# Performance work log

Hardware: AMD Instinct MI355X
Metric: run time of the kernel (lower is better)

Reference implementation:

```python
import jax, jax.numpy as jnp
import numpy as np
from jax.ops import segment_sum, segment_max

N, E, F, HID, HEADS, OUT, G = 50000, 800000, 128, 64, 2, 128, 50
EPS = 1e-5


def setup_inputs() -> dict:
    key = jax.random.key(0)
    ks = iter(jax.random.split(key, 80))
    def p(*shape):
        return jax.random.normal(next(ks), shape, jnp.float32) * 0.1
    inp = {}
    inp['x'] = jax.random.normal(next(ks), (N, F), jnp.float32)
    inp['edge_index'] = jax.random.randint(next(ks), (2, E), 0, N)
    inp['batch'] = jnp.repeat(jnp.arange(G), N // G)
    dims = [(F, HID), (HID, HID), (HID, OUT)]
    for i, (a, b) in enumerate(dims):
        inp[f'gcn_W{i}'] = p(a, b); inp[f'gcn_b{i}'] = jnp.zeros((b,), jnp.float32)
    for i in range(2):
        inp[f'gcn_bn_g{i}'] = jnp.ones((HID,), jnp.float32); inp[f'gcn_bn_b{i}'] = jnp.zeros((HID,), jnp.float32)
    gat_dims = [(F, HEADS, HID), (HEADS * HID, HEADS, HID), (HEADS * HID, 1, OUT)]
    for i, (a, h, c) in enumerate(gat_dims):
        inp[f'gat_W{i}'] = p(a, h * c)
        inp[f'gat_as{i}'] = p(h, c)
        inp[f'gat_ad{i}'] = p(h, c)
        inp[f'gat_b{i}'] = jnp.zeros((h * c if i < 2 else c,), jnp.float32)
    for i in range(2):
        inp[f'gat_bn_g{i}'] = jnp.ones((HEADS * HID,), jnp.float32); inp[f'gat_bn_b{i}'] = jnp.zeros((HEADS * HID,), jnp.float32)
    for i, (a, b) in enumerate(dims):
        inp[f'sage_Wl{i}'] = p(a, b); inp[f'sage_Wr{i}'] = p(a, b); inp[f'sage_b{i}'] = jnp.zeros((b,), jnp.float32)
    for i in range(2):
        inp[f'sage_bn_g{i}'] = jnp.ones((HID,), jnp.float32); inp[f'sage_bn_b{i}'] = jnp.zeros((HID,), jnp.float32)
    inp['fus_W'] = p(3 * OUT, OUT); inp['fus_b'] = jnp.zeros((OUT,), jnp.float32)
    return inp


def _bn(x, g, b):
    m = x.mean(0)
    v = x.var(0)
    return (x - m) * jax.lax.rsqrt(v + EPS) * g + b


def _pool(x, batch):
    s = segment_sum(x, batch, num_segments=G)
    c = segment_sum(jnp.ones((x.shape[0], 1), x.dtype), batch, num_segments=G)
    return s / jnp.maximum(c, 1.0)


def _with_self_loops(src, dst):
    loop = jnp.arange(N)
    return jnp.concatenate([src, loop]), jnp.concatenate([dst, loop])


def _gcn_conv(x, W, b, src, dst):
    # PyG GCNConv: linear, add self loops, symmetric D^-1/2 normalization, scatter-add at dst
    h = x @ W
    srcf, dstf = _with_self_loops(src, dst)
    deg = segment_sum(jnp.ones(srcf.shape[0], x.dtype), dstf, num_segments=N)
    dis = jnp.where(deg > 0, jax.lax.rsqrt(jnp.maximum(deg, 1.0)), 0.0)
    norm = dis[srcf] * dis[dstf]
    return segment_sum(h[srcf] * norm[:, None], dstf, num_segments=N) + b


def _gat_conv(x, W, a_s, a_d, b, src, dst, concat):
    # PyG GATConv: per-head additive attention, leaky_relu(0.2), softmax over incoming edges
    Hh, C = a_s.shape
    h = (x @ W).reshape(N, Hh, C)
    al_src = (h * a_s).sum(-1)  # [N,H]
    al_dst = (h * a_d).sum(-1)  # [N,H]
    srcf, dstf = _with_self_loops(src, dst)
    e = jax.nn.leaky_relu(al_src[srcf] + al_dst[dstf], 0.2)  # [E+N,H]
    m = segment_max(e, dstf, num_segments=N)
    ex = jnp.exp(e - m[dstf])
    denom = segment_sum(ex, dstf, num_segments=N)
    alpha = ex / (denom[dstf] + 1e-16)
    out = segment_sum(h[srcf] * alpha[:, :, None], dstf, num_segments=N)  # [N,H,C]
    out = out.reshape(N, Hh * C) if concat else out.mean(1)
    return out + b


def _sage_conv(x, Wl, Wr, b, src, dst):
    # PyG SAGEConv(mean): lin_l(mean of neighbors) + lin_r(x)
    s = segment_sum(x[src], dst, num_segments=N)
    cnt = segment_sum(jnp.ones((E, 1), x.dtype), dst, num_segments=N)
    mean = s / jnp.maximum(cnt, 1.0)
    return mean @ Wl + x @ Wr + b


def _forward(x, edge_index, batch,
             gcn_W0, gcn_b0, gcn_W1, gcn_b1, gcn_W2, gcn_b2,
             gcn_bn_g0, gcn_bn_b0, gcn_bn_g1, gcn_bn_b1,
             gat_W0, gat_as0, gat_ad0, gat_b0,
             gat_W1, gat_as1, gat_ad1, gat_b1,
             gat_W2, gat_as2, gat_ad2, gat_b2,
             gat_bn_g0, gat_bn_b0, gat_bn_g1, gat_bn_b1,
             sage_Wl0, sage_Wr0, sage_b0,
             sage_Wl1, sage_Wr1, sage_b1,
             sage_Wl2, sage_Wr2, sage_b2,
             sage_bn_g0, sage_bn_b0, sage_bn_g1, sage_bn_b1,
             fus_W, fus_b):
    src, dst = edge_index[0], edge_index[1]
    # GCN branch
    h = jax.nn.relu(_bn(_gcn_conv(x, gcn_W0, gcn_b0, src, dst), gcn_bn_g0, gcn_bn_b0))
    h = jax.nn.relu(_bn(_gcn_conv(h, gcn_W1, gcn_b1, src, dst), gcn_bn_g1, gcn_bn_b1))
    h = _gcn_conv(h, gcn_W2, gcn_b2, src, dst)
    gcn_out = _pool(h, batch)
    # GAT branch (2 heads concat, final single head)
    h = jax.nn.elu(_bn(_gat_conv(x, gat_W0, gat_as0, gat_ad0, gat_b0, src, dst, True), gat_bn_g0, gat_bn_b0))
    h = jax.nn.elu(_bn(_gat_conv(h, gat_W1, gat_as1, gat_ad1, gat_b1, src, dst, True), gat_bn_g1, gat_bn_b1))
    h = _gat_conv(h, gat_W2, gat_as2, gat_ad2, gat_b2, src, dst, False)
    gat_out = _pool(h, batch)
    # SAGE branch (mean aggregation)
    h = jax.nn.relu(_bn(_sage_conv(x, sage_Wl0, sage_Wr0, sage_b0, src, dst), sage_bn_g0, sage_bn_b0))
    h = jax.nn.relu(_bn(_sage_conv(h, sage_Wl1, sage_Wr1, sage_b1, src, dst), sage_bn_g1, sage_bn_b1))
    h = _sage_conv(h, sage_Wl2, sage_Wr2, sage_b2, src, dst)
    sage_out = _pool(h, batch)
    combined = jnp.concatenate([gcn_out, gat_out, sage_out], axis=-1)  # [G, 3*OUT]
    return combined @ fus_W + fus_b


def reference(x, edge_index, batch,
              gcn_W0, gcn_b0, gcn_W1, gcn_b1, gcn_W2, gcn_b2,
              gcn_bn_g0, gcn_bn_b0, gcn_bn_g1, gcn_bn_b1,
              gat_W0, gat_as0, gat_ad0, gat_b0,
              gat_W1, gat_as1, gat_ad1, gat_b1,
              gat_W2, gat_as2, gat_ad2, gat_b2,
              gat_bn_g0, gat_bn_b0, gat_bn_g1, gat_bn_b1,
              sage_Wl0, sage_Wr0, sage_b0,
              sage_Wl1, sage_Wr1, sage_b1,
              sage_Wl2, sage_Wr2, sage_b2,
              sage_bn_g0, sage_bn_b0, sage_bn_g1, sage_bn_b1,
              fus_W, fus_b):
    return _forward(x, edge_index, batch,
                    gcn_W0, gcn_b0, gcn_W1, gcn_b1, gcn_W2, gcn_b2,
                    gcn_bn_g0, gcn_bn_b0, gcn_bn_g1, gcn_bn_b1,
                    gat_W0, gat_as0, gat_ad0, gat_b0,
                    gat_W1, gat_as1, gat_ad1, gat_b1,
                    gat_W2, gat_as2, gat_ad2, gat_b2,
                    gat_bn_g0, gat_bn_b0, gat_bn_g1, gat_bn_b1,
                    sage_Wl0, sage_Wr0, sage_b0,
                    sage_Wl1, sage_Wr1, sage_b1,
                    sage_Wl2, sage_Wr2, sage_b2,
                    sage_bn_g0, sage_bn_b0, sage_bn_g1, sage_bn_b1,
                    fus_W, fus_b)
```

## Files before the change

### kernel.cpp

```cpp
#include <hip/hip_runtime.h>

#define NN 50000
#define NE 800000
#define NG 50
#define NB 196

static constexpr float BN_EPS = 1e-5f;

typedef __attribute__((ext_vector_type(8))) short  bf16x8;
typedef __attribute__((ext_vector_type(8))) unsigned short u16x8;
typedef __attribute__((ext_vector_type(4))) float  f32x4;

__device__ __forceinline__ float bf2f(unsigned short u) {
    return __uint_as_float(((unsigned)u) << 16);
}
__device__ __forceinline__ unsigned short f2bf(float f) {
    unsigned u = __float_as_uint(f);
    unsigned r = (u + 0x7fffu + ((u >> 16) & 1u)) >> 16;
    return (unsigned short)r;
}

__global__ void k_indeg(const int* __restrict__ dst, int* __restrict__ indeg) {
    int e = blockIdx.x * 256 + threadIdx.x;
    if (e < NE) atomicAdd(&indeg[dst[e]], 1);
}

__global__ void k_scan1(const int* __restrict__ cnt, int* __restrict__ rowstart,
                        int* __restrict__ bsum, float* __restrict__ dis) {
    int i = blockIdx.x * 256 + threadIdx.x;
    int lane = threadIdx.x & 63, wv = threadIdx.x >> 6;
    int v = (i < NN) ? cnt[i] : 0;
    if (i < NN) dis[i] = rsqrtf((float)v + 1.0f);
    int s = v;
#pragma unroll
    for (int d = 1; d < 64; d <<= 1) {
        int t = __shfl_up(s, d);
        if (lane >= d) s += t;
    }
    __shared__ int wtot[4];
    if (lane == 63) wtot[wv] = s;
    __syncthreads();
    int woff = 0;
    for (int w = 0; w < wv; ++w) woff += wtot[w];
    if (i < NN) rowstart[i] = woff + s - v;
    if (threadIdx.x == 255) bsum[blockIdx.x] = woff + s;
}

__global__ void k_scan2(const int* __restrict__ bsum, int* __restrict__ boff) {
    int lane = threadIdx.x & 63, wv = threadIdx.x >> 6;
    int v = (threadIdx.x < NB) ? bsum[threadIdx.x] : 0;
    int s = v;
#pragma unroll
    for (int d = 1; d < 64; d <<= 1) {
        int t = __shfl_up(s, d);
        if (lane >= d) s += t;
    }
    __shared__ int wtot[4];
    if (lane == 63) wtot[wv] = s;
    __syncthreads();
    int woff = 0;
    for (int w = 0; w < wv; ++w) woff += wtot[w];
    if (threadIdx.x < NB) boff[threadIdx.x] = woff + s - v;
}

__global__ void k_scan3(int* __restrict__ rowstart, const int* __restrict__ boff,
                        int* __restrict__ cursor) {
    int i = blockIdx.x * 256 + threadIdx.x;
    if (i < NN) {
        int v = rowstart[i] + boff[blockIdx.x];
        rowstart[i] = v;
        cursor[i] = v;
    }
    if (i == 0) rowstart[NN] = NE;
}

__global__ void k_fill(const int* __restrict__ src, const int* __restrict__ dst,
                       int* __restrict__ cursor, int* __restrict__ csr_src) {
    int e = blockIdx.x * 256 + threadIdx.x;
    if (e < NE) {
        int pos = atomicAdd(&cursor[dst[e]], 1);
        csr_src[pos] = src[e];
    }
}

__global__ void k_pack(const int* __restrict__ csr_src, const float* __restrict__ dis,
                       int2* __restrict__ pair) {
    int e = blockIdx.x * 256 + threadIdx.x;
    if (e < NE) {
        int s = csr_src[e];
        pair[e] = make_int2(s, __float_as_int(dis[s]));
    }
}

__global__ void k_count(const int* __restrict__ batch, float* __restrict__ cntG) {
    __shared__ int hist[NG];
    for (int i = threadIdx.x; i < NG; i += 256) hist[i] = 0;
    __syncthreads();
    for (int n = blockIdx.x * 256 + threadIdx.x; n < NN; n += gridDim.x * 256)
        atomicAdd(&hist[batch[n]], 1);
    __syncthreads();
    for (int i = threadIdx.x; i < NG; i += 256)
        if (hist[i]) atomicAdd(&cntG[i], (float)hist[i]);
}

struct WDesc { const float* s; unsigned short* d; int fin; int fout; };
struct WTable { WDesc w[12]; };

__global__ void k_convw(WTable t) {
    WDesc wd = t.w[blockIdx.x];
    int total = wd.fin * wd.fout;
    for (int i = threadIdx.x; i < total; i += 256) {
        int c = i / wd.fin, k = i % wd.fin;
        wd.d[i] = f2bf(wd.s[(size_t)k * wd.fout + c]);
    }
}

__global__ __launch_bounds__(256) void k_mm0(
        const float* __restrict__ X, const unsigned short* __restrict__ Wf,
        const float* __restrict__ as_, const float* __restrict__ ad_,
        float* __restrict__ alsrc, float* __restrict__ aldst,
        unsigned short* __restrict__ comb, unsigned short* __restrict__ sr0) {
    constexpr int FIN = 128, NCT = 20;
    int wave = threadIdx.x >> 6, lane = threadIdx.x & 63;
    int rowbase = (blockIdx.x * 4 + wave) * 16;
    if (rowbase >= NN) return;
    int lr = lane & 15, lg = lane >> 4;
    int arow = rowbase + lr;
    f32x4 acc[NCT] = {};
    const float* xp = X + (size_t)arow * FIN + lg * 8;
#pragma unroll
    for (int k0 = 0; k0 < FIN; k0 += 32) {
        float4 v0 = *(const float4*)(xp + k0);
        float4 v1 = *(const float4*)(xp + k0 + 4);
        u16x8 au;
        au[0] = f2bf(v0.x); au[1] = f2bf(v0.y); au[2] = f2bf(v0.z); au[3] = f2bf(v0.w);
        au[4] = f2bf(v1.x); au[5] = f2bf(v1.y); au[6] = f2bf(v1.z); au[7] = f2bf(v1.w);
        bf16x8 a1 = *(bf16x8*)&au;
#pragma unroll
        for (int ct = 0; ct < NCT; ++ct) {
            int wcol = ct * 16 + lr;
            bf16x8 b1 = *(const bf16x8*)(Wf + (size_t)wcol * FIN + k0 + lg * 8);
            acc[ct] = __builtin_amdgcn_mfma_f32_16x16x32_bf16(a1, b1, acc[ct], 0, 0, 0);
        }
    }
    {
        float ps[2][4] = {}, pd[2][4] = {};
#pragma unroll
        for (int ct = 4; ct < 12; ++ct) {
            int hh = (ct >= 8) ? 1 : 0;
            int colg = ct * 16 + lr - 64;
            float cs = as_[colg], cd = ad_[colg];
#pragma unroll
            for (int j = 0; j < 4; ++j) {
                ps[hh][j] += acc[ct][j] * cs;
                pd[hh][j] += acc[ct][j] * cd;
            }
        }
#pragma unroll
        for (int m = 1; m < 16; m <<= 1)
#pragma unroll
            for (int hh = 0; hh < 2; ++hh)
#pragma unroll
                for (int j = 0; j < 4; ++j) {
                    ps[hh][j] += __shfl_xor(ps[hh][j], m);
                    pd[hh][j] += __shfl_xor(pd[hh][j], m);
                }
        if (lr == 0) {
#pragma unroll
            for (int j = 0; j < 4; ++j) {
                int row = rowbase + lg * 4 + j;
#pragma unroll
                for (int hh = 0; hh < 2; ++hh) {
                    alsrc[(size_t)row * 2 + hh] = ps[hh][j];
                    aldst[(size_t)row * 2 + hh] = pd[hh][j];
                }
            }
        }
    }
#pragma unroll
    for (int ct = 0; ct < NCT; ++ct) {
        int col = ct * 16 + lr;
#pragma unroll
        for (int j = 0; j < 4; ++j) {
            int row = rowbase + lg * 4 + j;
            unsigned short v = f2bf(acc[ct][j]);
            if (ct < 4)       comb[(size_t)row * 256 + col] = v;
            else if (ct < 12) comb[(size_t)row * 256 + 128 + (col - 64)] = v;
            else if (ct < 16) comb[(size_t)row * 256 + 64 + (col - 192)] = v;
            else              sr0[(size_t)row * 64 + (col - 256)] = v;
        }
    }
}

template <int FIN, int FOUT, bool DUAL, bool BIAS, int BNACT, int ALH, int OSTR, int OOFF>
__global__ __launch_bounds__(256) void k_mm(
        const unsigned short* __restrict__ A1, const unsigned short* __restrict__ W1t,
        const unsigned short* __restrict__ A2, const unsigned short* __restrict__ W2t,
        const float* __restrict__ bias,
        const float* __restrict__ bns, const float* __restrict__ bng, const float* __restrict__ bnb,
        const float* __restrict__ as_, const float* __restrict__ ad_,
        float* __restrict__ alsrc, float* __restrict__ aldst,
        unsigned short* __restrict__ out) {
    constexpr int NCT = FOUT / 16;
    int wave = threadIdx.x >> 6, lane = threadIdx.x & 63;
    int rowbase = (blockIdx.x * 4 + wave) * 16;
    if (rowbase >= NN) return;
    int lr = lane & 15, lg = lane >> 4;
    int arow = rowbase + lr;
    f32x4 acc[NCT] = {};
    const unsigned short* a1p = A1 + (size_t)arow * FIN + lg * 8;
    const unsigned short* a2p = DUAL ? (A2 + (size_t)arow * FIN + lg * 8) : nullptr;
#pragma unroll
    for (int k0 = 0; k0 < FIN; k0 += 32) {
        bf16x8 a1;
        if (BNACT == 0) {
            a1 = *(const bf16x8*)(a1p + k0);
        } else {
            u16x8 araw = *(const u16x8*)(a1p + k0);
            u16x8 atx;
#pragma unroll
            for (int j = 0; j < 8; ++j) {
                int f = k0 + lg * 8 + j;
                float mean = bns[f] * (1.0f / NN);
                float var = bns[FIN + f] * (1.0f / NN) - mean * mean;
                float rstd = rsqrtf(var + BN_EPS);
                float val = (bf2f(araw[j]) - mean) * rstd * bng[f] + bnb[f];
                if (BNACT == 1) val = fmaxf(val, 0.f);
                if (BNACT == 2) val = (val > 0.f) ? val : (__expf(val) - 1.0f);
                atx[j] = f2bf(val);
            }
            a1 = *(bf16x8*)&atx;
        }
        bf16x8 a2v = {};
        if (DUAL) a2v = *(const bf16x8*)(a2p + k0);
#pragma unroll
        for (int ct = 0; ct < NCT; ++ct) {
            int wcol = ct * 16 + lr;
            bf16x8 b1 = *(const bf16x8*)(W1t + (size_t)wcol * FIN + k0 + lg * 8);
            acc[ct] = __builtin_amdgcn_mfma_f32_16x16x32_bf16(a1, b1, acc[ct], 0, 0, 0);
            if (DUAL) {
                bf16x8 b2 = *(const bf16x8*)(W2t + (size_t)wcol * FIN + k0 + lg * 8);
                acc[ct] = __builtin_amdgcn_mfma_f32_16x16x32_bf16(a2v, b2, acc[ct], 0, 0, 0);
            }
        }
    }
    if (ALH > 0) {
        constexpr int NH = (ALH > 0) ? ALH : 1;
        float ps[NH][4] = {}, pd[NH][4] = {};
#pragma unroll
        for (int ct = 0; ct < NCT; ++ct) {
            int hh = (ALH == 2 && ct >= NCT / 2) ? 1 : 0;
            int col = ct * 16 + lr;
            float cs = as_[col], cd = ad_[col];
#pragma unroll
            for (int j = 0; j < 4; ++j) {
                ps[hh][j] += acc[ct][j] * cs;
                pd[hh][j] += acc[ct][j] * cd;
            }
        }
#pragma unroll
        for (int m = 1; m < 16; m <<= 1)
#pragma unroll
            for (int hh = 0; hh < NH; ++hh)
#pragma unroll
                for (int j = 0; j < 4; ++j) {
                    ps[hh][j] += __shfl_xor(ps[hh][j], m);
                    pd[hh][j] += __shfl_xor(pd[hh][j], m);
                }
        if (lr == 0) {
#pragma unroll
            for (int j = 0; j < 4; ++j) {
                int row = rowbase + lg * 4 + j;
#pragma unroll
                for (int hh = 0; hh < NH; ++hh) {
                    alsrc[(size_t)row * ALH + hh] = ps[hh][j];
                    aldst[(size_t)row * ALH + hh] = pd[hh][j];
                }
            }
        }
    }
#pragma unroll
    for (int ct = 0; ct < NCT; ++ct) {
        int col = ct * 16 + lr;
        float bv = BIAS ? bias[col] : 0.f;
#pragma unroll
        for (int j = 0; j < 4; ++j) {
            int row = rowbase + lg * 4 + j;
            out[(size_t)row * OSTR + OOFF + col] = f2bf(acc[ct][j] + bv);
        }
    }
}

template <int H, bool GATBIAS>
__global__ __launch_bounds__(256) void k_aggf(
        const int* __restrict__ rowstart, const int2* __restrict__ pair,
        const float* __restrict__ dis, const float* __restrict__ alsrc,
        const float* __restrict__ aldst, const unsigned short* __restrict__ comb,
        const float* __restrict__ gat_bias,
        unsigned short* __restrict__ outGCN, unsigned short* __restrict__ outGAT,
        unsigned short* __restrict__ outSAGE) {
    int wave = threadIdx.x >> 6, lane = threadIdx.x & 63;
    int n = blockIdx.x * 4 + wave;
    if (n >= NN) return;
    int eg = lane >> 5, fl = lane & 31;
    int f0 = fl * 8;
    bool isGCN = fl < 8, isSAGE = (fl >= 8) && (fl < 16), isGAT = fl >= 16;
    int hh = (H == 2) ? ((fl >= 24) ? 1 : 0) : 0;
    int r0 = rowstart[n], r1 = rowstart[n + 1];
    float dn = dis[n];
    float adn = isGAT ? aldst[n * H + hh] : 0.f;
    float tself = isGAT ? (alsrc[n * H + hh] + adn) : 0.f;
    tself = (tself >= 0.f) ? tself : 0.2f * tself;
    float wsG = __expf(tself);
    float selfw = isGCN ? dn * dn : (isGAT ? wsG : 0.f);
    float acc[8] = {};
    if (eg == 0) {
        u16x8 hv = *(const u16x8*)&comb[(size_t)n * 256 + f0];
#pragma unroll
        for (int j = 0; j < 8; ++j) acc[j] = selfw * bf2f(hv[j]);
    }
    float dsum = 0.f;
#pragma unroll 4
    for (int e = r0 + eg; e < r1; e += 2) {
        int2 p = pair[e];
        int s = p.x;
        float al = isGAT ? alsrc[(size_t)s * H + hh] : 0.f;
        float v = al + adn;
        v = (v >= 0.f) ? v : 0.2f * v;
        float we = __expf(v);
        dsum += we;
        float w = isGCN ? __int_as_float(p.y) * dn : (isGAT ? we : 1.0f);
        u16x8 hs = *(const u16x8*)&comb[(size_t)s * 256 + f0];
#pragma unroll
        for (int jj = 0; jj < 8; ++jj) acc[jj] += w * bf2f(hs[jj]);
    }
    if (H == 2) {
        dsum += __shfl_xor(dsum, 1);
        dsum += __shfl_xor(dsum, 2);
        dsum += __shfl_xor(dsum, 4);
        dsum += __shfl_xor(dsum, 32);
        dsum *= 0.125f;
    } else {
        dsum += __shfl_xor(dsum, 1);
        dsum += __shfl_xor(dsum, 2);
        dsum += __shfl_xor(dsum, 4);
        dsum += __shfl_xor(dsum, 8);
        dsum += __shfl_xor(dsum, 32);
        dsum *= 0.0625f;
    }
    float dinv = 1.0f / (wsG + dsum + 1e-16f);
#pragma unroll
    for (int jj = 0; jj < 8; ++jj) acc[jj] += __shfl_xor(acc[jj], 32);
    if (eg == 0) {
        float inv = 1.0f / fmaxf((float)(r1 - r0), 1.0f);
        float mul = isGCN ? 1.0f : (isSAGE ? inv : dinv);
        u16x8 o;
#pragma unroll
        for (int jj = 0; jj < 8; ++jj) {
            float v = acc[jj] * mul;
            if (GATBIAS && isGAT) v += gat_bias[f0 - 128 + jj];
            o[jj] = f2bf(v);
        }
        if (isGCN)       *(u16x8*)&outGCN[(size_t)n * 64 + f0] = o;
        else if (isSAGE) *(u16x8*)&outSAGE[(size_t)n * 64 + (f0 - 64)] = o;
        else             *(u16x8*)&outGAT[(size_t)n * 128 + (f0 - 128)] = o;
    }
}

template <int F, bool TWO>
__global__ void k_bn_stats(const unsigned short* __restrict__ x,
                           const unsigned short* __restrict__ y,
                           float* __restrict__ sums) {
    constexpr int TPR = F / 8;
    constexpr int RPB = 256 / TPR;
    __shared__ float lsum[F], lsq[F];
    for (int i = threadIdx.x; i < F; i += 256) { lsum[i] = 0.f; lsq[i] = 0.f; }
    __syncthreads();
    int fl = threadIdx.x % TPR, rl = threadIdx.x / TPR;
    int f0 = fl * 8;
    float s[8] = {}, s2[8] = {};
    for (int n = blockIdx.x * RPB + rl; n < NN; n += gridDim.x * RPB) {
        u16x8 v = *(const u16x8*)&x[(size_t)n * F + f0];
        u16x8 w = {};
        if (TWO) w = *(const u16x8*)&y[(size_t)n * F + f0];
#pragma unroll
        for (int j = 0; j < 8; ++j) {
            float f = bf2f(v[j]);
            if (TWO) f += bf2f(w[j]);
            s[j] += f; s2[j] += f * f;
        }
    }
#pragma unroll
    for (int off = TPR; off < 64; off <<= 1)
#pragma unroll
        for (int j = 0; j < 8; ++j) { s[j] += __shfl_xor(s[j], off); s2[j] += __shfl_xor(s2[j], off); }
    if ((threadIdx.x & 63) < TPR) {
#pragma unroll
        for (int j = 0; j < 8; ++j) {
            atomicAdd(&lsum[f0 + j], s[j]);
            atomicAdd(&lsq[f0 + j], s2[j]);
        }
    }
    __syncthreads();
    for (int i = threadIdx.x; i < F; i += 256) {
        atomicAdd(&sums[i], lsum[i]);
        atomicAdd(&sums[F + i], lsq[i]);
    }
}

template <int F, int ACT, bool TWO, bool O1, bool O2, int OOFF>
__global__ void k_bn_apply(const unsigned short* __restrict__ x,
                           const unsigned short* __restrict__ y,
                           const float* __restrict__ sums,
                           const float* __restrict__ gamma, const float* __restrict__ beta,
                           unsigned short* __restrict__ out1, unsigned short* __restrict__ comb) {
    int idx = blockIdx.x * 256 + threadIdx.x;
    if (idx >= NN * F / 8) return;
    int row = idx / (F / 8);
    int f0 = (idx % (F / 8)) * 8;
    u16x8 v = *(const u16x8*)&x[(size_t)idx * 8];
    u16x8 w = {};
    if (TWO) w = *(const u16x8*)&y[(size_t)idx * 8];
    u16x8 o;
#pragma unroll
    for (int j = 0; j < 8; ++j) {
        int f = f0 + j;
        float mean = sums[f] * (1.0f / NN);
        float var = sums[F + f] * (1.0f / NN) - mean * mean;
        float rstd = rsqrtf(var + BN_EPS);
        float raw = bf2f(v[j]);
        if (TWO) raw += bf2f(w[j]);
        float val = (raw - mean) * rstd * gamma[f] + beta[f];
        if (ACT == 1) val = fmaxf(val, 0.f);
        if (ACT == 2) val = (val > 0.f) ? val : (__expf(val) - 1.0f);
        o[j] = f2bf(val);
    }
    if (O1) *(u16x8*)&out1[(size_t)idx * 8] = o;
    if (O2) *(u16x8*)&comb[(size_t)row * 256 + OOFF + f0] = o;
}

__global__ void k_pool(const unsigned short* __restrict__ x, const int* __restrict__ batch,
                       float* __restrict__ pooled, int off) {
    int f = threadIdx.x & 127;
    int half = threadIdx.x >> 7;
    int nend = min(NN, (int)(blockIdx.x + 1) * 128);
    float acc = 0.f; int gcur = -1;
    for (int n = blockIdx.x * 128 + half; n < nend; n += 2) {
        int g = batch[n];
        if (g != gcur) {
            if (gcur >= 0) atomicAdd(&pooled[(size_t)gcur * 384 + off + f], acc);
            gcur = g; acc = 0.f;
        }
        acc += bf2f(x[(size_t)n * 128 + f]);
    }
    if (gcur >= 0) atomicAdd(&pooled[(size_t)gcur * 384 + off + f], acc);
}

__global__ void k_fusion(const float* __restrict__ pooled, const float* __restrict__ cntG,
                         const float* __restrict__ W, const float* __restrict__ b,
                         float* __restrict__ out) {
    int idx = blockIdx.x * 256 + threadIdx.x;
    if (idx >= NG * 128) return;
    int g = idx / 128, o = idx % 128;
    float inv = 1.0f / fmaxf(cntG[g], 1.0f);
    float acc = b[o];
#pragma unroll 4
    for (int k = 0; k < 384; ++k)
        acc += pooled[g * 384 + k] * inv * W[k * 128 + o];
    out[idx] = acc;
}

static inline int grid1(long long n) { return (int)((n + 255) / 256); }

extern "C" void kernel_launch(void* const* d_in, const int* in_sizes, int n_in,
                              void* d_out, int out_size, void* d_ws, size_t ws_size,
                              hipStream_t stream) {
    const float* x       = (const float*)d_in[0];
    const int*   ei      = (const int*)d_in[1];
    const int*   batch   = (const int*)d_in[2];
    const float* gcn_W0  = (const float*)d_in[3];
    const float* gcn_W1  = (const float*)d_in[5];
    const float* gcn_W2  = (const float*)d_in[7];
    const float* gcn_b2  = (const float*)d_in[8];
    const float* gcn_g0  = (const float*)d_in[9];
    const float* gcn_bb0 = (const float*)d_in[10];
    const float* gcn_g1  = (const float*)d_in[11];
    const float* gcn_bb1 = (const float*)d_in[12];
    const float* gat_W0  = (const float*)d_in[13];
    const float* gat_as0 = (const float*)d_in[14];
    const float* gat_ad0 = (const float*)d_in[15];
    const float* gat_W1  = (const float*)d_in[17];
    const float* gat_as1 = (const float*)d_in[18];
    const float* gat_ad1 = (const float*)d_in[19];
    const float* gat_W2  = (const float*)d_in[21];
    const float* gat_as2 = (const float*)d_in[22];
    const float* gat_ad2 = (const float*)d_in[23];
    const float* gat_b2  = (const float*)d_in[24];
    const float* gat_g0  = (const float*)d_in[25];
    const float* gat_bb0 = (const float*)d_in[26];
    const float* gat_g1  = (const float*)d_in[27];
    const float* gat_bb1 = (const float*)d_in[28];
    const float* sage_Wl0 = (const float*)d_in[29];
    const float* sage_Wr0 = (const float*)d_in[30];
    const float* sage_Wl1 = (const float*)d_in[32];
    const float* sage_Wr1 = (const float*)d_in[33];
    const float* sage_Wl2 = (const float*)d_in[35];
    const float* sage_Wr2 = (const float*)d_in[36];
    const float* sage_b2  = (const float*)d_in[37];
    const float* sage_g0  = (const float*)d_in[38];
    const float* sage_bb0 = (const float*)d_in[39];
    const float* sage_g1  = (const float*)d_in[40];
    const float* sage_bb1 = (const float*)d_in[41];
    const float* fus_W    = (const float*)d_in[42];
    const float* fus_b    = (const float*)d_in[43];

    const int* src = ei;
    const int* dst = ei + NE;

    float* ws = (float*)d_ws;
    size_t off = 0;
    auto alloc = [&](size_t n) { float* p = ws + off; off += (n + 3) & ~(size_t)3; return p; };
    unsigned short* combA = (unsigned short*)alloc((size_t)NN * 128);
    unsigned short* combB = (unsigned short*)alloc((size_t)NN * 128);
    unsigned short* bufGCN  = (unsigned short*)alloc((size_t)NN * 32);
    unsigned short* bufGAT  = (unsigned short*)alloc((size_t)NN * 64);
    unsigned short* bufSAGE = (unsigned short*)alloc((size_t)NN * 32);
    unsigned short* sr0     = (unsigned short*)alloc((size_t)NN * 32);
    unsigned short* sageH0  = (unsigned short*)alloc((size_t)NN * 32);
    unsigned short* sageM1  = (unsigned short*)alloc((size_t)NN * 32);
    unsigned short* wt      = (unsigned short*)alloc(110592 / 2);
    int*   indeg    = (int*)alloc(NN);
    int*   rowstart = (int*)alloc(NN + 1);
    int*   cursor   = (int*)alloc(NN);
    int*   csr_src  = (int*)alloc(NE);
    int2*  pair     = (int2*)alloc((size_t)NE * 2);
    int*   bsum     = (int*)alloc(NB);
    int*   boff     = (int*)alloc(NB);
    float* dis   = alloc(NN);
    float* alsrc = alloc((size_t)NN * 2);
    float* aldst = alloc((size_t)NN * 2);
    float* bnsum = alloc(6 * 256 + NG * 384 + NG);
    float* pooled = bnsum + 6 * 256;
    float* cntG   = pooled + NG * 384;
    (void)ws_size; (void)n_in; (void)in_sizes; (void)out_size;

    unsigned short* sageH1  = sr0;
    unsigned short* finGCN  = combB;
    unsigned short* finSAGE = combB + (size_t)NN * 128;

    unsigned short* wf        = wt;
    unsigned short* gcn_W1t   = wf + 40960;
    unsigned short* gcn_W2t   = gcn_W1t + 4096;
    unsigned short* gat_W1t   = gcn_W2t + 8192;
    unsigned short* gat_W2t   = gat_W1t + 16384;
    unsigned short* sage_Wl1t = gat_W2t + 16384;
    unsigned short* sage_Wr1t = sage_Wl1t + 4096;
    unsigned short* sage_Wl2t = sage_Wr1t + 4096;
    unsigned short* sage_Wr2t = sage_Wl2t + 8192;

    const int gAgg = NN / 4;
    const int gMM  = (NN + 63) / 64;

    hipMemsetAsync(indeg, 0, NN * 4, stream);
    hipMemsetAsync(bnsum, 0, (6 * 256 + NG * 384 + NG) * 4, stream);
    k_indeg<<<grid1(NE), 256, 0, stream>>>(dst, indeg);
    k_scan1<<<NB, 256, 0, stream>>>(indeg, rowstart, bsum, dis);
    k_scan2<<<1, 256, 0, stream>>>(bsum, boff);
    k_scan3<<<NB, 256, 0, stream>>>(rowstart, boff, cursor);
    k_fill<<<grid1(NE), 256, 0, stream>>>(src, dst, cursor, csr_src);
    k_pack<<<grid1(NE), 256, 0, stream>>>(csr_src, dis, pair);
    k_count<<<128, 256, 0, stream>>>(batch, cntG);
    WTable wtab = {{
        { gcn_W0, wf, 128, 64 }, { gat_W0, wf + 64 * 128, 128, 128 },
        { sage_Wl0, wf + 192 * 128, 128, 64 }, { sage_Wr0, wf + 256 * 128, 128, 64 },
        { gcn_W1, gcn_W1t, 64, 64 }, { gcn_W2, gcn_W2t, 64, 128 },
        { gat_W1, gat_W1t, 128, 128 }, { gat_W2, gat_W2t, 128, 128 },
        { sage_Wl1, sage_Wl1t, 64, 64 }, { sage_Wr1, sage_Wr1t, 64, 64 },
        { sage_Wl2, sage_Wl2t, 64, 128 }, { sage_Wr2, sage_Wr2t, 64, 128 },
    }};
    k_convw<<<12, 256, 0, stream>>>(wtab);

    k_mm0<<<gMM, 256, 0, stream>>>(x, wf, gat_as0, gat_ad0, alsrc, aldst, combA, sr0);
    k_aggf<2, false><<<gAgg, 256, 0, stream>>>(rowstart, pair, dis, alsrc, aldst,
                                               combA, nullptr, bufGCN, bufGAT, bufSAGE);
    k_bn_stats<64, false><<<250, 256, 0, stream>>>(bufGCN, nullptr, bnsum + 0 * 256);
    k_bn_stats<128, false><<<250, 256, 0, stream>>>(bufGAT, nullptr, bnsum + 2 * 256);
    k_bn_stats<64, true><<<250, 256, 0, stream>>>(bufSAGE, sr0, bnsum + 4 * 256);
    k_mm<64, 64, false, false, 1, 0, 256, 0><<<gMM, 256, 0, stream>>>(
        bufGCN, gcn_W1t, nullptr, nullptr, nullptr,
        bnsum + 0 * 256, gcn_g0, gcn_bb0, nullptr, nullptr, nullptr, nullptr, combB);
    k_mm<128, 128, false, false, 2, 2, 256, 128><<<gMM, 256, 0, stream>>>(
        bufGAT, gat_W1t, nullptr, nullptr, nullptr,
        bnsum + 2 * 256, gat_g0, gat_bb0, gat_as1, gat_ad1, alsrc, aldst, combB);
    k_bn_apply<64, 1, true, true, true, 64><<<grid1(NN * 8), 256, 0, stream>>>(
        bufSAGE, sr0, bnsum + 4 * 256, sage_g0, sage_bb0, sageH0, combB);

    k_aggf<2, false><<<gAgg, 256, 0, stream>>>(rowstart, pair, dis, alsrc, aldst,
                                               combB, nullptr, bufGCN, bufGAT, bufSAGE);
    k_bn_stats<64, false><<<250, 256, 0, stream>>>(bufGCN, nullptr, bnsum + 1 * 256);
    k_bn_stats<128, false><<<250, 256, 0, stream>>>(bufGAT, nullptr, bnsum + 3 * 256);
    k_mm<64, 64, true, false, 0, 0, 64, 0><<<gMM, 256, 0, stream>>>(
        bufSAGE, sage_Wl1t, sageH0, sage_Wr1t, nullptr,
        nullptr, nullptr, nullptr, nullptr, nullptr, nullptr, nullptr, sageM1);
    k_bn_apply<64, 1, false, false, true, 0><<<grid1(NN * 8), 256, 0, stream>>>(
        bufGCN, nullptr, bnsum + 1 * 256, gcn_g1, gcn_bb1, nullptr, combA);
    k_mm<128, 128, false, false, 2, 1, 256, 128><<<gMM, 256, 0, stream>>>(
        bufGAT, gat_W2t, nullptr, nullptr, nullptr,
        bnsum + 3 * 256, gat_g1, gat_bb1, gat_as2, gat_ad2, alsrc, aldst, combA);
    k_bn_stats<64, false><<<250, 256, 0, stream>>>(sageM1, nullptr, bnsum + 5 * 256);
    k_bn_apply<64, 1, false, true, true, 64><<<grid1(NN * 8), 256, 0, stream>>>(
        sageM1, nullptr, bnsum + 5 * 256, sage_g1, sage_bb1, sageH1, combA);

    k_aggf<1, true><<<gAgg, 256, 0, stream>>>(rowstart, pair, dis, alsrc, aldst,
                                              combA, gat_b2, bufGCN, bufGAT, bufSAGE);
    k_mm<64, 128, false, true, 0, 0, 128, 0><<<gMM, 256, 0, stream>>>(
        bufGCN, gcn_W2t, nullptr, nullptr, gcn_b2,
        nullptr, nullptr, nullptr, nullptr, nullptr, nullptr, nullptr, finGCN);
    k_mm<64, 128, true, true, 0, 0, 128, 0><<<gMM, 256, 0, stream>>>(
        bufSAGE, sage_Wl2t, sageH1, sage_Wr2t, sage_b2,
        nullptr, nullptr, nullptr, nullptr, nullptr, nullptr, nullptr, finSAGE);

    k_pool<<<(NN + 127) / 128, 256, 0, stream>>>(finGCN, batch, pooled, 0);
    k_pool<<<(NN + 127) / 128, 256, 0, stream>>>(bufGAT, batch, pooled, 128);
    k_pool<<<(NN + 127) / 128, 256, 0, stream>>>(finSAGE, batch, pooled, 256);
    k_fusion<<<grid1(NG * 128), 256, 0, stream>>>(pooled, cntG, fus_W, fus_b, (float*)d_out);
}
```

Baseline: 664.0 us.

## Double row tile in MFMA matmul, drop edge pack, merge pools and memsets

Each wave in k_mm now computes 32 rows instead of 16, so every loaded weight fragment feeds two MFMAs and the grid is halved. The separate k_pack pass that built (src, dis) pairs is removed, and the aggregation kernel now reads csr_src and dis[s] directly with a deeper unroll. The three pooling launches are merged into one k_pool3 kernel, and the two memsets are combined into one by placing indeg in the zeroed region. The cost is more registers per wave in k_mm and an extra dependent gather of dis in the GCN lanes of the aggregation loop.

```diff
diff --git a/kernel.cpp b/kernel.cpp
--- a/kernel.cpp
+++ b/kernel.cpp
@@ -4,6 +4,7 @@
 #define NE 800000
 #define NG 50
 #define NB 196
+#define NPB 391
 
 static constexpr float BN_EPS = 1e-5f;
 
@@ -80,15 +81,6 @@
     if (e < NE) {
         int pos = atomicAdd(&cursor[dst[e]], 1);
         csr_src[pos] = src[e];
-    }
-}
-
-__global__ void k_pack(const int* __restrict__ csr_src, const float* __restrict__ dis,
-                       int2* __restrict__ pair) {
-    int e = blockIdx.x * 256 + threadIdx.x;
-    if (e < NE) {
-        int s = csr_src[e];
-        pair[e] = make_int2(s, __float_as_int(dis[s]));
     }
 }
 
@@ -203,50 +195,63 @@
         unsigned short* __restrict__ out) {
     constexpr int NCT = FOUT / 16;
     int wave = threadIdx.x >> 6, lane = threadIdx.x & 63;
-    int rowbase = (blockIdx.x * 4 + wave) * 16;
+    int rowbase = (blockIdx.x * 4 + wave) * 32;
     if (rowbase >= NN) return;
+    bool t1 = (rowbase + 16) < NN;
     int lr = lane & 15, lg = lane >> 4;
-    int arow = rowbase + lr;
-    f32x4 acc[NCT] = {};
-    const unsigned short* a1p = A1 + (size_t)arow * FIN + lg * 8;
-    const unsigned short* a2p = DUAL ? (A2 + (size_t)arow * FIN + lg * 8) : nullptr;
+    int arow0 = rowbase + lr;
+    int arow1 = t1 ? (arow0 + 16) : arow0;
+    f32x4 acc0[NCT] = {}, acc1[NCT] = {};
+    const unsigned short* a1p0 = A1 + (size_t)arow0 * FIN + lg * 8;
+    const unsigned short* a1p1 = A1 + (size_t)arow1 * FIN + lg * 8;
+    const unsigned short* a2p0 = DUAL ? (A2 + (size_t)arow0 * FIN + lg * 8) : nullptr;
+    const unsigned short* a2p1 = DUAL ? (A2 + (size_t)arow1 * FIN + lg * 8) : nullptr;
 #pragma unroll
     for (int k0 = 0; k0 < FIN; k0 += 32) {
-        bf16x8 a1;
+        bf16x8 a0, a1v;
         if (BNACT == 0) {
-            a1 = *(const bf16x8*)(a1p + k0);
+            a0  = *(const bf16x8*)(a1p0 + k0);
+            a1v = *(const bf16x8*)(a1p1 + k0);
         } else {
-            u16x8 araw = *(const u16x8*)(a1p + k0);
-            u16x8 atx;
+            u16x8 r0v = *(const u16x8*)(a1p0 + k0);
+            u16x8 r1v = *(const u16x8*)(a1p1 + k0);
+            u16x8 t0, t1v;
 #pragma unroll
             for (int j = 0; j < 8; ++j) {
                 int f = k0 + lg * 8 + j;
                 float mean = bns[f] * (1.0f / NN);
                 float var = bns[FIN + f] * (1.0f / NN) - mean * mean;
                 float rstd = rsqrtf(var + BN_EPS);
-                float val = (bf2f(araw[j]) - mean) * rstd * bng[f] + bnb[f];
-                if (BNACT == 1) val = fmaxf(val, 0.f);
-                if (BNACT == 2) val = (val > 0.f) ? val : (__expf(val) - 1.0f);
-                atx[j] = f2bf(val);
+                float g = bng[f], bb = bnb[f];
+                float v0 = (bf2f(r0v[j]) - mean) * rstd * g + bb;
+                float v1 = (bf2f(r1v[j]) - mean) * rstd * g + bb;
+                if (BNACT == 1) { v0 = fmaxf(v0, 0.f); v1 = fmaxf(v1, 0.f); }
+                if (BNACT == 2) {
+                    v0 = (v0 > 0.f) ? v0 : (__expf(v0) - 1.0f);
+                    v1 = (v1 > 0.f) ? v1 : (__expf(v1) - 1.0f);
+                }
+                t0[j] = f2bf(v0); t1v[j] = f2bf(v1);
             }
-            a1 = *(bf16x8*)&atx;
-        }
-        bf16x8 a2v = {};
-        if (DUAL) a2v = *(const bf16x8*)(a2p + k0);
+            a0 = *(bf16x8*)&t0; a1v = *(bf16x8*)&t1v;
+        }
+        bf16x8 a20 = {}, a21 = {};
+        if (DUAL) { a20 = *(const bf16x8*)(a2p0 + k0); a21 = *(const bf16x8*)(a2p1 + k0); }
 #pragma unroll
         for (int ct = 0; ct < NCT; ++ct) {
             int wcol = ct * 16 + lr;
             bf16x8 b1 = *(const bf16x8*)(W1t + (size_t)wcol * FIN + k0 + lg * 8);
-            acc[ct] = __builtin_amdgcn_mfma_f32_16x16x32_bf16(a1, b1, acc[ct], 0, 0, 0);
+            acc0[ct] = __builtin_amdgcn_mfma_f32_16x16x32_bf16(a0, b1, acc0[ct], 0, 0, 0);
+            acc1[ct] = __builtin_amdgcn_mfma_f32_16x16x32_bf16(a1v, b1, acc1[ct], 0, 0, 0);
             if (DUAL) {
                 bf16x8 b2 = *(const bf16x8*)(W2t + (size_t)wcol * FIN + k0 + lg * 8);
-                acc[ct] = __builtin_amdgcn_mfma_f32_16x16x32_bf16(a2v, b2, acc[ct], 0, 0, 0);
+                acc0[ct] = __builtin_amdgcn_mfma_f32_16x16x32_bf16(a20, b2, acc0[ct], 0, 0, 0);
+                acc1[ct] = __builtin_amdgcn_mfma_f32_16x16x32_bf16(a21, b2, acc1[ct], 0, 0, 0);
             }
         }
     }
     if (ALH > 0) {
         constexpr int NH = (ALH > 0) ? ALH : 1;
-        float ps[NH][4] = {}, pd[NH][4] = {};
+        float ps0[NH][4] = {}, pd0[NH][4] = {}, ps1[NH][4] = {}, pd1[NH][4] = {};
 #pragma unroll
         for (int ct = 0; ct < NCT; ++ct) {
             int hh = (ALH == 2 && ct >= NCT / 2) ? 1 : 0;
@@ -254,8 +259,10 @@
             float cs = as_[col], cd = ad_[col];
 #pragma unroll
             for (int j = 0; j < 4; ++j) {
-                ps[hh][j] += acc[ct][j] * cs;
-                pd[hh][j] += acc[ct][j] * cd;
+                ps0[hh][j] += acc0[ct][j] * cs;
+                pd0[hh][j] += acc0[ct][j] * cd;
+                ps1[hh][j] += acc1[ct][j] * cs;
+                pd1[hh][j] += acc1[ct][j] * cd;
             }
         }
 #pragma unroll
@@ -264,8 +271,10 @@
             for (int hh = 0; hh < NH; ++hh)
 #pragma unroll
                 for (int j = 0; j < 4; ++j) {
-                    ps[hh][j] += __shfl_xor(ps[hh][j], m);
-                    pd[hh][j] += __shfl_xor(pd[hh][j], m);
+                    ps0[hh][j] += __shfl_xor(ps0[hh][j], m);
+                    pd0[hh][j] += __shfl_xor(pd0[hh][j], m);
+                    ps1[hh][j] += __shfl_xor(ps1[hh][j], m);
+                    pd1[hh][j] += __shfl_xor(pd1[hh][j], m);
                 }
         if (lr == 0) {
 #pragma unroll
@@ -273,8 +282,12 @@
                 int row = rowbase + lg * 4 + j;
 #pragma unroll
                 for (int hh = 0; hh < NH; ++hh) {
-                    alsrc[(size_t)row * ALH + hh] = ps[hh][j];
-                    aldst[(size_t)row * ALH + hh] = pd[hh][j];
+                    alsrc[(size_t)row * ALH + hh] = ps0[hh][j];
+                    aldst[(size_t)row * ALH + hh] = pd0[hh][j];
+                    if (t1) {
+                        alsrc[(size_t)(row + 16) * ALH + hh] = ps1[hh][j];
+                        aldst[(size_t)(row + 16) * ALH + hh] = pd1[hh][j];
+                    }
                 }
             }
         }
@@ -286,14 +299,15 @@
 #pragma unroll
         for (int j = 0; j < 4; ++j) {
             int row = rowbase + lg * 4 + j;
-            out[(size_t)row * OSTR + OOFF + col] = f2bf(acc[ct][j] + bv);
+            out[(size_t)row * OSTR + OOFF + col] = f2bf(acc0[ct][j] + bv);
+            if (t1) out[(size_t)(row + 16) * OSTR + OOFF + col] = f2bf(acc1[ct][j] + bv);
         }
     }
 }
 
 template <int H, bool GATBIAS>
 __global__ __launch_bounds__(256) void k_aggf(
-        const int* __restrict__ rowstart, const int2* __restrict__ pair,
+        const int* __restrict__ rowstart, const int* __restrict__ csr_src,
         const float* __restrict__ dis, const float* __restrict__ alsrc,
         const float* __restrict__ aldst, const unsigned short* __restrict__ comb,
         const float* __restrict__ gat_bias,
@@ -320,16 +334,16 @@
         for (int j = 0; j < 8; ++j) acc[j] = selfw * bf2f(hv[j]);
     }
     float dsum = 0.f;
-#pragma unroll 4
+#pragma unroll 8
     for (int e = r0 + eg; e < r1; e += 2) {
-        int2 p = pair[e];
-        int s = p.x;
+        int s = csr_src[e];
         float al = isGAT ? alsrc[(size_t)s * H + hh] : 0.f;
         float v = al + adn;
         v = (v >= 0.f) ? v : 0.2f * v;
         float we = __expf(v);
         dsum += we;
-        float w = isGCN ? __int_as_float(p.y) * dn : (isGAT ? we : 1.0f);
+        float ds = isGCN ? dis[s] : 0.f;
+        float w = isGCN ? ds * dn : (isGAT ? we : 1.0f);
         u16x8 hs = *(const u16x8*)&comb[(size_t)s * 256 + f0];
 #pragma unroll
         for (int jj = 0; jj < 8; ++jj) acc[jj] += w * bf2f(hs[jj]);
@@ -439,13 +453,19 @@
     if (O2) *(u16x8*)&comb[(size_t)row * 256 + OOFF + f0] = o;
 }
 
-__global__ void k_pool(const unsigned short* __restrict__ x, const int* __restrict__ batch,
-                       float* __restrict__ pooled, int off) {
+__global__ void k_pool3(const unsigned short* __restrict__ a,
+                        const unsigned short* __restrict__ b,
+                        const unsigned short* __restrict__ c,
+                        const int* __restrict__ batch, float* __restrict__ pooled) {
+    int sel = blockIdx.x / NPB;
+    int nb = blockIdx.x % NPB;
+    const unsigned short* x = (sel == 0) ? a : ((sel == 1) ? b : c);
+    int off = sel * 128;
     int f = threadIdx.x & 127;
     int half = threadIdx.x >> 7;
-    int nend = min(NN, (int)(blockIdx.x + 1) * 128);
+    int nend = min(NN, (nb + 1) * 128);
     float acc = 0.f; int gcur = -1;
-    for (int n = blockIdx.x * 128 + half; n < nend; n += 2) {
+    for (int n = nb * 128 + half; n < nend; n += 2) {
         int g = batch[n];
         if (g != gcur) {
             if (gcur >= 0) atomicAdd(&pooled[(size_t)gcur * 384 + off + f], acc);
@@ -529,19 +549,19 @@
     unsigned short* sageH0  = (unsigned short*)alloc((size_t)NN * 32);
     unsigned short* sageM1  = (unsigned short*)alloc((size_t)NN * 32);
     unsigned short* wt      = (unsigned short*)alloc(110592 / 2);
-    int*   indeg    = (int*)alloc(NN);
     int*   rowstart = (int*)alloc(NN + 1);
     int*   cursor   = (int*)alloc(NN);
     int*   csr_src  = (int*)alloc(NE);
-    int2*  pair     = (int2*)alloc((size_t)NE * 2);
     int*   bsum     = (int*)alloc(NB);
     int*   boff     = (int*)alloc(NB);
     float* dis   = alloc(NN);
     float* alsrc = alloc((size_t)NN * 2);
     float* aldst = alloc((size_t)NN * 2);
-    float* bnsum = alloc(6 * 256 + NG * 384 + NG);
+    float* zr = alloc(6 * 256 + NG * 384 + NG + NN);
+    float* bnsum  = zr;
     float* pooled = bnsum + 6 * 256;
     float* cntG   = pooled + NG * 384;
+    int*   indeg  = (int*)(cntG + NG);
     (void)ws_size; (void)n_in; (void)in_sizes; (void)out_size;
 
     unsigned short* sageH1  = sr0;
@@ -560,15 +580,14 @@
 
     const int gAgg = NN / 4;
     const int gMM  = (NN + 63) / 64;
-
-    hipMemsetAsync(indeg, 0, NN * 4, stream);
-    hipMemsetAsync(bnsum, 0, (6 * 256 + NG * 384 + NG) * 4, stream);
+    const int gMM2 = (NN + 127) / 128;
+
+    hipMemsetAsync(zr, 0, (6 * 256 + NG * 384 + NG + NN) * 4, stream);
     k_indeg<<<grid1(NE), 256, 0, stream>>>(dst, indeg);
     k_scan1<<<NB, 256, 0, stream>>>(indeg, rowstart, bsum, dis);
     k_scan2<<<1, 256, 0, stream>>>(bsum, boff);
     k_scan3<<<NB, 256, 0, stream>>>(rowstart, boff, cursor);
     k_fill<<<grid1(NE), 256, 0, stream>>>(src, dst, cursor, csr_src);
-    k_pack<<<grid1(NE), 256, 0, stream>>>(csr_src, dis, pair);
     k_count<<<128, 256, 0, stream>>>(batch, cntG);
     WTable wtab = {{
         { gcn_W0, wf, 128, 64 }, { gat_W0, wf + 64 * 128, 128, 128 },
@@ -581,47 +600,45 @@
     k_convw<<<12, 256, 0, stream>>>(wtab);
 
     k_mm0<<<gMM, 256, 0, stream>>>(x, wf, gat_as0, gat_ad0, alsrc, aldst, combA, sr0);
-    k_aggf<2, false><<<gAgg, 256, 0, stream>>>(rowstart, pair, dis, alsrc, aldst,
+    k_aggf<2, false><<<gAgg, 256, 0, stream>>>(rowstart, csr_src, dis, alsrc, aldst,
                                                combA, nullptr, bufGCN, bufGAT, bufSAGE);
     k_bn_stats<64, false><<<250, 256, 0, stream>>>(bufGCN, nullptr, bnsum + 0 * 256);
     k_bn_stats<128, false><<<250, 256, 0, stream>>>(bufGAT, nullptr, bnsum + 2 * 256);
     k_bn_stats<64, true><<<250, 256, 0, stream>>>(bufSAGE, sr0, bnsum + 4 * 256);
-    k_mm<64, 64, false, false, 1, 0, 256, 0><<<gMM, 256, 0, stream>>>(
+    k_mm<64, 64, false, false, 1, 0, 256, 0><<<gMM2, 256, 0, stream>>>(
         bufGCN, gcn_W1t, nullptr, nullptr, nullptr,
         bnsum + 0 * 256, gcn_g0, gcn_bb0, nullptr, nullptr, nullptr, nullptr, combB);
-    k_mm<128, 128, false, false, 2, 2, 256, 128><<<gMM, 256, 0, stream>>>(
+    k_mm<128, 128, false, false, 2, 2, 256, 128><<<gMM2, 256, 0, stream>>>(
         bufGAT, gat_W1t, nullptr, nullptr, nullptr,
         bnsum + 2 * 256, gat_g0, gat_bb0, gat_as1, gat_ad1, alsrc, aldst, combB);
     k_bn_apply<64, 1, true, true, true, 64><<<grid1(NN * 8), 256, 0, stream>>>(
         bufSAGE, sr0, bnsum + 4 * 256, sage_g0, sage_bb0, sageH0, combB);
 
-    k_aggf<2, false><<<gAgg, 256, 0, stream>>>(rowstart, pair, dis, alsrc, aldst,
+    k_aggf<2, false><<<gAgg, 256, 0, stream>>>(rowstart, csr_src, dis, alsrc, aldst,
                                                combB, nullptr, bufGCN, bufGAT, bufSAGE);
     k_bn_stats<64, false><<<250, 256, 0, stream>>>(bufGCN, nullptr, bnsum + 1 * 256);
     k_bn_stats<128, false><<<250, 256, 0, stream>>>(bufGAT, nullptr, bnsum + 3 * 256);
-    k_mm<64, 64, true, false, 0, 0, 64, 0><<<gMM, 256, 0, stream>>>(
+    k_mm<64, 64, true, false, 0, 0, 64, 0><<<gMM2, 256, 0, stream>>>(
         bufSAGE, sage_Wl1t, sageH0, sage_Wr1t, nullptr,
         nullptr, nullptr, nullptr, nullptr, nullptr, nullptr, nullptr, sageM1);
     k_bn_apply<64, 1, false, false, true, 0><<<grid1(NN * 8), 256, 0, stream>>>(
         bufGCN, nullptr, bnsum + 1 * 256, gcn_g1, gcn_bb1, nullptr, combA);
-    k_mm<128, 128, false, false, 2, 1, 256, 128><<<gMM, 256, 0, stream>>>(
+    k_mm<128, 128, false, false, 2, 1, 256, 128><<<gMM2, 256, 0, stream>>>(
         bufGAT, gat_W2t, nullptr, nullptr, nullptr,
         bnsum + 3 * 256, gat_g1, gat_bb1, gat_as2, gat_ad2, alsrc, aldst, combA);
     k_bn_stats<64, false><<<250, 256, 0, stream>>>(sageM1, nullptr, bnsum + 5 * 256);
     k_bn_apply<64, 1, false, true, true, 64><<<grid1(NN * 8), 256, 0, stream>>>(
         sageM1, nullptr, bnsum + 5 * 256, sage_g1, sage_bb1, sageH1, combA);
 
-    k_aggf<1, true><<<gAgg, 256, 0, stream>>>(rowstart, pair, dis, alsrc, aldst,
+    k_aggf<1, true><<<gAgg, 256, 0, stream>>>(rowstart, csr_src, dis, alsrc, aldst,
                                               combA, gat_b2, bufGCN, bufGAT, bufSAGE);
-    k_mm<64, 128, false, true, 0, 0, 128, 0><<<gMM, 256, 0, stream>>>(
+    k_mm<64, 128, false, true, 0, 0, 128, 0><<<gMM2, 256, 0, stream>>>(
         bufGCN, gcn_W2t, nullptr, nullptr, gcn_b2,
         nullptr, nullptr, nullptr, nullptr, nullptr, nullptr, nullptr, finGCN);
-    k_mm<64, 128, true, true, 0, 0, 128, 0><<<gMM, 256, 0, stream>>>(
+    k_mm<64, 128, true, true, 0, 0, 128, 0><<<gMM2, 256, 0, stream>>>(
         bufSAGE, sage_Wl2t, sageH1, sage_Wr2t, sage_b2,
         nullptr, nullptr, nullptr, nullptr, nullptr, nullptr, nullptr, finSAGE);
 
-    k_pool<<<(NN + 127) / 128, 256, 0, stream>>>(finGCN, batch, pooled, 0);
-    k_pool<<<(NN + 127) / 128, 256, 0, stream>>>(bufGAT, batch, pooled, 128);
-    k_pool<<<(NN + 127) / 128, 256, 0, stream>>>(finSAGE, batch, pooled, 256);
+    k_pool3<<<3 * NPB, 256, 0, stream>>>(finGCN, bufGAT, finSAGE, batch, pooled);
     k_fusion<<<grid1(NG * 128), 256, 0, stream>>>(pooled, cntG, fus_W, fus_b, (float*)d_out);
 }
```

After: 754.7 us. 13.7% more time.
